# Kernel optimization log

Hardware: AMD Instinct MI355X
Metric: run time of the kernel (lower is better)

## Reference

```python
import math
import jax, jax.numpy as jnp
import numpy as np

B, C, NH, H, W = 8, 512, 4, 64, 64
CH = C // 8          # qkv channels = 64
HC = CH // NH        # head channels = 16


def _pos_encoding(c, h, w):
    # Faithful to torch code, including the raw memory reinterpretation of
    # pos_h (h, c) -> (1, c, h, 1) and pos_w (c//2, 2w) -> (1, c, 1, w).
    ph = jnp.arange(h, dtype=jnp.float32)[:, None]            # (h, 1)
    pw = jnp.arange(w, dtype=jnp.float32)[None, :]            # (1, w)
    div = jnp.exp(jnp.arange(0, c, 2, dtype=jnp.float32) * (-(math.log(10000.0) / c)))
    pos_h = ph * div[None, :]                                  # (h, c/2)
    pos_w = pw * div[:, None]                                  # (c/2, w)
    pos_h = jnp.concatenate([jnp.sin(pos_h), jnp.cos(pos_h)], axis=1)  # (h, c)
    pos_w = jnp.concatenate([jnp.sin(pos_w), jnp.cos(pos_w)], axis=1)  # (c/2, 2w)
    pos_h = pos_h.reshape(1, c, h, 1)   # raw view, as in torch
    pos_w = pos_w.reshape(1, c, 1, w)   # raw view, as in torch
    return pos_h + pos_w                # (1, c, h, w)


def _conv1x1(x, w, b):
    return jnp.einsum('bchw,oc->bohw', x, w) + b[None, :, None, None]


def setup_inputs() -> dict:
    key = jax.random.key(0)
    ks = jax.random.split(key, 6)
    s = 0.02
    return {
        'x':  jax.random.normal(ks[0], (B, C, H, W), dtype=jnp.float32),
        'wq': jax.random.normal(ks[1], (CH, C), dtype=jnp.float32) * s,
        'bq': jnp.zeros((CH,), dtype=jnp.float32),
        'wk': jax.random.normal(ks[2], (CH, C), dtype=jnp.float32) * s,
        'bk': jnp.zeros((CH,), dtype=jnp.float32),
        'wv': jax.random.normal(ks[3], (CH, C), dtype=jnp.float32) * s,
        'bv': jnp.zeros((CH,), dtype=jnp.float32),
        'wo': jax.random.normal(ks[4], (C, CH), dtype=jnp.float32) * s,
        'bo': jnp.zeros((C,), dtype=jnp.float32),
        'gamma': jnp.full((1,), 0.5, dtype=jnp.float32),  # nonzero to exercise whole graph
    }


def reference(x, wq, bq, wk, bk, wv, bv, wo, bo, gamma):
    b, c, h, w = x.shape
    nh, hc = NH, HC
    x = x + _pos_encoding(c, h, w)

    q = _conv1x1(x, wq, bq).reshape(b, nh, hc, h, w)
    k = _conv1x1(x, wk, bk).reshape(b, nh, hc, h, w)
    v = _conv1x1(x, wv, bv).reshape(b, nh, hc, h, w)

    # column (H) and row (W) views
    q_H = q.transpose(0, 1, 4, 2, 3).reshape(b * nh * w, hc, h).transpose(0, 2, 1)  # (bnw, h, hc)
    q_W = q.transpose(0, 1, 3, 2, 4).reshape(b * nh * h, hc, w).transpose(0, 2, 1)  # (bnh, w, hc)
    k_H = k.transpose(0, 1, 4, 2, 3).reshape(b * nh * w, hc, h)
    k_W = k.transpose(0, 1, 3, 2, 4).reshape(b * nh * h, hc, w)
    v_H = v.transpose(0, 1, 4, 2, 3).reshape(b * nh * w, hc, h)
    v_W = v.transpose(0, 1, 3, 2, 4).reshape(b * nh * h, hc, w)

    inf_mask = jnp.where(jnp.eye(h, dtype=bool), -jnp.inf, 0.0).astype(x.dtype)  # (h, h)
    energy_H = (jnp.matmul(q_H, k_H) + inf_mask[None]).reshape(b, nh, w, h, h).transpose(0, 2, 1, 3, 4)  # (b,w,nh,h,h)
    energy_W = jnp.matmul(q_W, k_W).reshape(b, nh, h, w, w).transpose(0, 2, 1, 3, 4)                     # (b,h,nh,w,w)

    conc = jax.nn.softmax(jnp.concatenate([energy_H, energy_W], axis=4), axis=4)  # (b,w,nh,h,h+w)

    att_H = conc[..., :h].transpose(0, 2, 1, 3, 4).reshape(b * nh * w, h, h)
    # NOTE: faithful to torch: (b,h,nh,w,w) is flattened in (b,h,nh) order
    att_W = conc[..., h:h + w].reshape(b * nh * h, w, w)

    out_H = jnp.matmul(v_H, att_H.transpose(0, 2, 1))
    out_H = out_H.reshape(b, nh, w, hc, h).transpose(0, 3, 4, 1, 2).reshape(b, nh * hc, h, w)
    out_W = jnp.matmul(v_W, att_W.transpose(0, 2, 1))
    out_W = out_W.reshape(b, nh, h, hc, w).transpose(0, 3, 1, 4, 2).reshape(b, nh * hc, h, w)

    out = _conv1x1(out_H + out_W, wo, bo)
    return gamma * out + x
```

## Files before the change

kernel.cpp:

```cpp
#include <hip/hip_runtime.h>
#include <math.h>


typedef unsigned int u32;
typedef unsigned short u16;
typedef __attribute__((ext_vector_type(8))) short short8;
typedef __attribute__((ext_vector_type(4))) float f32x4;

__device__ __forceinline__ u16 f2bf(float v) {
    u32 u = __float_as_uint(v);
    u32 r = (u + 0x7FFFu + ((u >> 16) & 1u)) >> 16;
    return (u16)r;
}

__device__ __forceinline__ float bf2f(u16 v) {
    return __uint_as_float(((u32)v) << 16);
}

__device__ __forceinline__ void gll16(const void* g, void* l) {
    __builtin_amdgcn_global_load_lds(
        (const __attribute__((address_space(1))) u32*)g,
        (__attribute__((address_space(3))) u32*)l, 16, 0, 0);
}

__global__ __launch_bounds__(64) void pos_kernel(float* __restrict__ PH,
                                                 float* __restrict__ PW) {
    const float r = 0.03597789207798663f;
    int c = blockIdx.x;
    int t = threadIdx.x;
    int i = c >> 3;
    int j = ((c & 7) << 6) | t;
    float ph;
    if (j < 256) ph = sinf((float)i * expf(-(float)j * r));
    else         ph = cosf((float)i * expf(-(float)(j - 256) * r));
    PH[c * 64 + t] = ph;
    int tt = c >> 1;
    float dv = expf(-(float)tt * r);
    PW[c * 64 + t] = (c & 1) ? cosf((float)t * dv) : sinf((float)t * dv);
}

__global__ __launch_bounds__(256) void wconv_kernel(
    const float* __restrict__ wq, const float* __restrict__ wk,
    const float* __restrict__ wv, const float* __restrict__ wo,
    u16* __restrict__ WT, u16* __restrict__ WOb) {
    int i = blockIdx.x * 256 + threadIdx.x;
    if (i < 98304) {
        float v;
        if (i < 32768)      v = wq[i];
        else if (i < 65536) v = wk[i - 32768];
        else                v = wv[i - 65536];
        WT[i] = f2bf(v);
    } else {
        WOb[i - 98304] = f2bf(wo[i - 98304]);
    }
}

__global__ __launch_bounds__(256) void wpos_kernel(
    const float* __restrict__ wq, const float* __restrict__ wk,
    const float* __restrict__ wv,
    const float* __restrict__ PH, const float* __restrict__ PW,
    float* __restrict__ WPH3, float* __restrict__ WPW3) {
    int gid = blockIdx.x * 256 + threadIdx.x;
    int h = gid & 63;
    int m = (gid >> 6) & 63;
    int t = gid >> 12;
    int mg = t >> 1, tbl = t & 1;
    const float* W = (mg == 0) ? wq : (mg == 1) ? wk : wv;
    const float* P = tbl ? PW : PH;
    const float* wr = W + m * 512;
    float s = 0.f;
#pragma unroll 8
    for (int c = 0; c < 512; ++c) s += wr[c] * P[c * 64 + h];
    (tbl ? WPW3 : WPH3)[(mg * 64 + m) * 64 + h] = s;
}

__global__ __launch_bounds__(512, 4) void qkvx_kernel(
    const float* __restrict__ x, const u16* __restrict__ WT,
    const float* __restrict__ bq, const float* __restrict__ bk,
    const float* __restrict__ bv,
    const float* __restrict__ WPH3, const float* __restrict__ WPW3,
    u16* __restrict__ Qc, u16* __restrict__ Kc, u16* __restrict__ Vc) {
    __shared__ u16 Wb[192 * 64];
    __shared__ u16 Bb[64 * 64];
    int L  = blockIdx.x;
    int b  = L & 7;
    int pt = L >> 3;
    int tid  = threadIdx.x;
    int w    = tid >> 6;
    int lane = tid & 63;
    int ln15 = lane & 15, quad = lane >> 4;
    int wm = w >> 2;
    int wp = w & 3;

    f32x4 acc[6];
#pragma unroll
    for (int i = 0; i < 6; ++i) acc[i] = (f32x4){0.f, 0.f, 0.f, 0.f};

    const float* xb = x + (size_t)b * 2097152 + pt * 64;
    int tp  = tid & 63;
    int tcc = tid >> 6;

    for (int kc = 0; kc < 512; kc += 64) {
        __syncthreads();
#pragma unroll
        for (int it = 0; it < 3; ++it) {
            int idx = tid + it * 512;
            int r = idx >> 3, s = idx & 7;
            gll16(WT + r * 512 + kc + ((s ^ (r & 7)) * 8), &Wb[idx * 8]);
        }
        {
            const float* xp = xb + (size_t)(kc + tcc * 8) * 4096 + tp;
            float v[8];
#pragma unroll
            for (int i = 0; i < 8; ++i) v[i] = xp[(size_t)i * 4096];
            short8 pk;
#pragma unroll
            for (int i = 0; i < 8; ++i) pk[i] = (short)f2bf(v[i]);
            *(short8*)&Bb[tp * 64 + ((tcc ^ (tp & 7)) * 8)] = pk;
        }
        __syncthreads();
#pragma unroll
        for (int ks = 0; ks < 2; ++ks) {
            int cs = ks * 4 + quad;
            int brow = wp * 16 + ln15;
            short8 bf = *(const short8*)&Bb[brow * 64 + ((cs ^ (brow & 7)) * 8)];
#pragma unroll
            for (int i = 0; i < 6; ++i) {
                int arow = (wm * 6 + i) * 16 + ln15;
                short8 af = *(const short8*)&Wb[arow * 64 + ((cs ^ (arow & 7)) * 8)];
                acc[i] = __builtin_amdgcn_mfma_f32_16x16x32_bf16(
                    af, bf, acc[i], 0, 0, 0);
            }
        }
    }

    int wc = wp * 16 + ln15;
#pragma unroll
    for (int i = 0; i < 6; ++i) {
        int mf = wm * 6 + i;
        int mg = mf >> 2, nm = mf & 3;
        const float* bias = (mg == 0) ? bq : (mg == 1) ? bk : bv;
        u16* T = (mg == 0) ? Qc : (mg == 1) ? Kc : Vc;
        float vals[4];
#pragma unroll
        for (int reg = 0; reg < 4; ++reg) {
            int m2 = nm * 16 + quad * 4 + reg;
            vals[reg] = acc[i][reg] + bias[m2]
                      + WPH3[(mg * 64 + m2) * 64 + pt]
                      + WPW3[(mg * 64 + m2) * 64 + wc];
        }
        ushort4 pk;
        pk.x = f2bf(vals[0]);
        pk.y = f2bf(vals[1]);
        pk.z = f2bf(vals[2]);
        pk.w = f2bf(vals[3]);
        *(ushort4*)&T[(((size_t)(b * 4 + nm) * 64 + pt) * 64 + wc) * 16
                      + quad * 4] = pk;
    }
}

__global__ __launch_bounds__(256, 4) void attn_kernel(
    const u16* __restrict__ Qc, const u16* __restrict__ Kc,
    const u16* __restrict__ Vc,
    u16* __restrict__ OHc, u16* __restrict__ OWc) {
    __shared__ u16 U[11008];
    u16* A_lds  = U;
    u16* B_lds  = U + 2560;
    u16* P_lds  = U;
    u16* VH_lds = U + 8704;
    u16* VW_lds = U + 9856;

    int b = blockIdx.x, n = blockIdx.y, a = blockIdx.z;
    int tid  = threadIdx.x;
    int w    = tid >> 6;
    int lane = tid & 63;
    int ln15 = lane & 15, quad = lane >> 4;
    int nv = a >> 4;
    int hv = ((a & 15) << 2) | n;

    const size_t cb = (((size_t)b * 4 + n) * 64 + a) * 1024;

    {
        int t = tid & 127;
        const short8 z8 = {0, 0, 0, 0, 0, 0, 0, 0};
        if (tid < 128) {
            int h = t >> 1, half = t & 1;
            size_t hb = (((size_t)b * 4 + n) * 64 + h) * 1024 + a * 16 + half * 8;
            short8 vA = *(const short8*)(Qc + hb);
            *(short8*)&A_lds[h * 40 + half * 8] = vA;
            short8 vK = *(const short8*)(Kc + hb);
            *(short8*)&B_lds[h * 48 + half * 8] = vK;
            *(short8*)&B_lds[h * 48 + 16 + half * 8] = z8;
            short8 vV = *(const short8*)(Vc + hb);
#pragma unroll
            for (int j = 0; j < 8; ++j)
                VH_lds[(half * 8 + j) * 72 + h] = (u16)vV[j];
        } else {
            short8 vA = *(const short8*)(Qc + cb + t * 8);
            *(short8*)&A_lds[(t >> 1) * 40 + 16 + (t & 1) * 8] = vA;
            short8 vK = *(const short8*)(Kc + cb + t * 8);
            *(short8*)&B_lds[(64 + (t >> 1)) * 48 + 16 + (t & 1) * 8] = vK;
            *(short8*)&B_lds[(64 + (t >> 1)) * 48 + (t & 1) * 8] = z8;
            size_t wb2 = (((size_t)b * 4 + nv) * 64 + hv) * 1024 + t * 8;
            short8 vV = *(const short8*)(Vc + wb2);
#pragma unroll
            for (int j = 0; j < 8; ++j)
                VW_lds[((t & 1) * 8 + j) * 72 + (t >> 1)] = (u16)vV[j];
        }
    }
    __syncthreads();

    const f32x4 zf = {0.f, 0.f, 0.f, 0.f};
    short8 af = *(const short8*)&A_lds[(w * 16 + ln15) * 40 + quad * 8];
    f32x4 acc[8];
#pragma unroll
    for (int nt = 0; nt < 8; ++nt) {
        short8 bf = *(const short8*)&B_lds[(nt * 16 + ln15) * 48 + quad * 8];
        acc[nt] = __builtin_amdgcn_mfma_f32_16x16x32_bf16(af, bf, zf, 0, 0, 0);
    }

#pragma unroll
    for (int nt = 0; nt < 4; ++nt)
#pragma unroll
        for (int r = 0; r < 4; ++r)
            if (nt * 16 + ln15 == w * 16 + quad * 4 + r) acc[nt][r] = -1e30f;

    float inv[4];
#pragma unroll
    for (int r = 0; r < 4; ++r) {
        float mrow = acc[0][r];
#pragma unroll
        for (int nt = 1; nt < 8; ++nt) mrow = fmaxf(mrow, acc[nt][r]);
        mrow = fmaxf(mrow, __shfl_xor(mrow, 1, 64));
        mrow = fmaxf(mrow, __shfl_xor(mrow, 2, 64));
        mrow = fmaxf(mrow, __shfl_xor(mrow, 4, 64));
        mrow = fmaxf(mrow, __shfl_xor(mrow, 8, 64));
        float s = 0.f;
#pragma unroll
        for (int nt = 0; nt < 8; ++nt) {
            float e = __expf(acc[nt][r] - mrow);
            acc[nt][r] = e;
            s += e;
        }
        s += __shfl_xor(s, 1, 64);
        s += __shfl_xor(s, 2, 64);
        s += __shfl_xor(s, 4, 64);
        s += __shfl_xor(s, 8, 64);
        inv[r] = 1.0f / s;
    }
    __syncthreads();
#pragma unroll
    for (int nt = 0; nt < 8; ++nt)
#pragma unroll
        for (int r = 0; r < 4; ++r)
            P_lds[(w * 16 + quad * 4 + r) * 136 + nt * 16 + ln15] =
                f2bf(acc[nt][r] * inv[r]);
    __syncthreads();

    int prow = (w * 16 + ln15) * 136;
    short8 a0 = *(const short8*)&P_lds[prow +       quad * 8];
    short8 a1 = *(const short8*)&P_lds[prow + 32  + quad * 8];
    short8 a2 = *(const short8*)&P_lds[prow + 64  + quad * 8];
    short8 a3 = *(const short8*)&P_lds[prow + 96  + quad * 8];
    short8 b0 = *(const short8*)&VH_lds[ln15 * 72 +      quad * 8];
    short8 b1 = *(const short8*)&VH_lds[ln15 * 72 + 32 + quad * 8];
    short8 c0 = *(const short8*)&VW_lds[ln15 * 72 +      quad * 8];
    short8 c1 = *(const short8*)&VW_lds[ln15 * 72 + 32 + quad * 8];
    f32x4 oH = __builtin_amdgcn_mfma_f32_16x16x32_bf16(a0, b0, zf, 0, 0, 0);
    oH = __builtin_amdgcn_mfma_f32_16x16x32_bf16(a1, b1, oH, 0, 0, 0);
    f32x4 oW = __builtin_amdgcn_mfma_f32_16x16x32_bf16(a2, c0, zf, 0, 0, 0);
    oW = __builtin_amdgcn_mfma_f32_16x16x32_bf16(a3, c1, oW, 0, 0, 0);

    __syncthreads();
    u16* eph = U;
    u16* epw = U + 16 * 68;
#pragma unroll
    for (int r = 0; r < 4; ++r) {
        eph[(quad * 4 + r) * 68 + ln15 * 4 + w]   = f2bf(oH[r]);
        epw[(w * 16 + quad * 4 + r) * 20 + ln15]  = f2bf(oW[r]);
    }
    __syncthreads();
    {
        int t = tid;
        ushort4 vh = *(const ushort4*)&eph[(t >> 4) * 68 + (t & 15) * 4];
        ushort4 vw = *(const ushort4*)&epw[(t >> 2) * 20 + (t & 3) * 4];
        size_t cbase = (((size_t)b * 4 + n) * 64 + a) * 1024;
        *(ushort4*)&OHc[cbase + t * 4] = vh;
        *(ushort4*)&OWc[cbase + t * 4] = vw;
    }
}

__global__ __launch_bounds__(256) void sconv_kernel(
    const u16* __restrict__ OHc, const u16* __restrict__ OWc,
    u16* __restrict__ Sb) {
    int b = blockIdx.x;
    int h = blockIdx.y;
    int t  = threadIdx.x;
    int wp = t >> 2;
    int cq = t & 3;

    const u16* ohp = OHc + ((((size_t)b * 4 + (h & 3)) * 64 + wp) * 1024
                            + (h >> 2) * 64 + cq * 16);
    short8 oh0 = *(const short8*)ohp;
    short8 oh1 = *(const short8*)(ohp + 8);

    const u16* owb = OWc + (((size_t)b * 4 + (wp & 3)) * 64) * 1024 + h * 16 + cq * 4;
    ushort4 owv[4];
#pragma unroll
    for (int nvi = 0; nvi < 4; ++nvi)
        owv[nvi] = *(const ushort4*)(owb + (size_t)((nvi << 4) | (wp >> 2)) * 1024);

    u16 res[16];
#pragma unroll
    for (int j = 0; j < 16; ++j) {
        u16 ohv = (j < 8) ? (u16)oh0[j] : (u16)oh1[j - 8];
        const ushort4& q = owv[j & 3];
        u16 owu = (j >> 2) == 0 ? q.x : (j >> 2) == 1 ? q.y : (j >> 2) == 2 ? q.z : q.w;
        res[j] = f2bf(bf2f(ohv) + bf2f(owu));
    }
    u16* dst = Sb + (((size_t)b * 4096 + h * 64 + wp) * 64 + cq * 16);
    *(short8*)dst       = *(short8*)&res[0];
    *(short8*)(dst + 8) = *(short8*)&res[8];
}

__global__ __launch_bounds__(256, 4) void finalm_kernel(
    const u16* __restrict__ Sb, const u16* __restrict__ WOb,
    const float* __restrict__ bo, const float* __restrict__ gamma,
    const float* __restrict__ x, const float* __restrict__ PH,
    const float* __restrict__ PW, float* __restrict__ out) {
    __shared__ u16 Ab[64 * 64];
    __shared__ u16 Bb[128 * 64];
    int pt = blockIdx.x;
    int mc = blockIdx.y;
    int b  = blockIdx.z;
    int tid  = threadIdx.x;
    int w    = tid >> 6;
    int lane = tid & 63;
    int ln15 = lane & 15, quad = lane >> 4;
    int p0 = pt * 128, m0 = mc * 64;

    float4 xv[4][2];
#pragma unroll
    for (int mf = 0; mf < 4; ++mf) {
        int m = m0 + mf * 16 + ln15;
#pragma unroll
        for (int pf = 0; pf < 2; ++pf) {
            int pb = p0 + w * 32 + pf * 16 + quad * 4;
            xv[mf][pf] = *(const float4*)&x[((size_t)(b * 512 + m)) * 4096 + pb];
        }
    }

    const u16* Ag = WOb + m0 * 64;
    const u16* Sg = Sb + ((size_t)b * 4096 + p0) * 64;

#pragma unroll
    for (int it = 0; it < 2; ++it) {
        int idx = tid + it * 256;
        int r = idx >> 3, s = idx & 7;
        gll16(Ag + r * 64 + ((s ^ (r & 7)) * 8), &Ab[idx * 8]);
    }
#pragma unroll
    for (int it = 0; it < 4; ++it) {
        int idx = tid + it * 256;
        int r = idx >> 3, s = idx & 7;
        gll16(Sg + r * 64 + ((s ^ (r & 7)) * 8), &Bb[idx * 8]);
    }
    __syncthreads();

    const f32x4 zf = {0.f, 0.f, 0.f, 0.f};
    f32x4 acc[4][2];
#pragma unroll
    for (int mf = 0; mf < 4; ++mf)
#pragma unroll
        for (int pf = 0; pf < 2; ++pf)
            acc[mf][pf] = zf;
#pragma unroll
    for (int ks = 0; ks < 2; ++ks) {
        int cs = ks * 4 + quad;
        short8 af[2], bf[4];
#pragma unroll
        for (int pf = 0; pf < 2; ++pf) {
            int row = w * 32 + pf * 16 + ln15;
            af[pf] = *(const short8*)&Bb[row * 64 + ((cs ^ (row & 7)) * 8)];
        }
#pragma unroll
        for (int mf = 0; mf < 4; ++mf) {
            int row = mf * 16 + ln15;
            bf[mf] = *(const short8*)&Ab[row * 64 + ((cs ^ (row & 7)) * 8)];
        }
#pragma unroll
        for (int mf = 0; mf < 4; ++mf)
#pragma unroll
            for (int pf = 0; pf < 2; ++pf)
                acc[mf][pf] = __builtin_amdgcn_mfma_f32_16x16x32_bf16(
                    af[pf], bf[mf], acc[mf][pf], 0, 0, 0);
    }

    float g = gamma[0];
    int h = pt * 2 + (w >> 1);
    int plb = (w & 1) * 32;
#pragma unroll
    for (int mf = 0; mf < 4; ++mf) {
        int m = m0 + mf * 16 + ln15;
        float bm = bo[m];
        float ph = PH[m * 64 + h];
#pragma unroll
        for (int pf = 0; pf < 2; ++pf) {
            int pb = p0 + w * 32 + pf * 16 + quad * 4;
            size_t o = ((size_t)(b * 512 + m)) * 4096 + pb;
            float4 pwv = *(const float4*)&PW[m * 64 + plb + pf * 16 + quad * 4];
            float4 res;
            res.x = g * (acc[mf][pf][0] + bm) + xv[mf][pf].x + ph + pwv.x;
            res.y = g * (acc[mf][pf][1] + bm) + xv[mf][pf].y + ph + pwv.y;
            res.z = g * (acc[mf][pf][2] + bm) + xv[mf][pf].z + ph + pwv.z;
            res.w = g * (acc[mf][pf][3] + bm) + xv[mf][pf].w + ph + pwv.w;
            *(float4*)&out[o] = res;
        }
    }
}

extern "C" void kernel_launch(void* const* d_in, const int* in_sizes, int n_in,
                              void* d_out, int out_size, void* d_ws, size_t ws_size,
                              hipStream_t stream) {
    const float* x     = (const float*)d_in[0];
    const float* wq    = (const float*)d_in[1];
    const float* bq    = (const float*)d_in[2];
    const float* wk    = (const float*)d_in[3];
    const float* bk    = (const float*)d_in[4];
    const float* wv    = (const float*)d_in[5];
    const float* bv    = (const float*)d_in[6];
    const float* wo    = (const float*)d_in[7];
    const float* bo    = (const float*)d_in[8];
    const float* gamma = (const float*)d_in[9];
    float* out = (float*)d_out;
    float* ws  = (float*)d_ws;

    float* PH   = ws;
    float* PW   = PH + 32768;
    float* WPH3 = PW + 32768;
    float* WPW3 = WPH3 + 12288;
    u16*   WT   = (u16*)(WPW3 + 12288);
    u16*   WOb  = WT + 98304;
    u16*   Qc   = WOb + 32768;
    u16*   Kc   = Qc + 2097152;
    u16*   Vc   = Kc + 2097152;
    u16*   OHc  = Vc + 2097152;
    u16*   OWc  = OHc + 2097152;
    u16*   Sbb  = OWc + 2097152;

    pos_kernel<<<dim3(512), dim3(64), 0, stream>>>(PH, PW);
    wconv_kernel<<<dim3(512), dim3(256), 0, stream>>>(wq, wk, wv, wo, WT, WOb);
    wpos_kernel<<<dim3(96), dim3(256), 0, stream>>>(wq, wk, wv, PH, PW, WPH3, WPW3);
    qkvx_kernel<<<dim3(512), dim3(512), 0, stream>>>(
        x, WT, bq, bk, bv, WPH3, WPW3, Qc, Kc, Vc);
    attn_kernel<<<dim3(8, 4, 64), dim3(256), 0, stream>>>(
        Qc, Kc, Vc, OHc, OWc);
    sconv_kernel<<<dim3(8, 64), dim3(256), 0, stream>>>(OHc, OWc, Sbb);
    finalm_kernel<<<dim3(32, 8, 8), dim3(256), 0, stream>>>(
        Sbb, WOb, bo, gamma, x, PH, PW, out);
}
```

Before: 197.2 us.

## Fuse head-sum into final projection and merge prep kernels

Result: no change. 196.6 us (-0.3%).

```diff
diff --git a/kernel.cpp b/kernel.cpp
--- a/kernel.cpp
+++ b/kernel.cpp
@@ -23,35 +23,37 @@
         (__attribute__((address_space(3))) u32*)l, 16, 0, 0);
 }
 
-__global__ __launch_bounds__(64) void pos_kernel(float* __restrict__ PH,
-                                                 float* __restrict__ PW) {
-    const float r = 0.03597789207798663f;
-    int c = blockIdx.x;
-    int t = threadIdx.x;
-    int i = c >> 3;
-    int j = ((c & 7) << 6) | t;
-    float ph;
-    if (j < 256) ph = sinf((float)i * expf(-(float)j * r));
-    else         ph = cosf((float)i * expf(-(float)(j - 256) * r));
-    PH[c * 64 + t] = ph;
-    int tt = c >> 1;
-    float dv = expf(-(float)tt * r);
-    PW[c * 64 + t] = (c & 1) ? cosf((float)t * dv) : sinf((float)t * dv);
-}
-
-__global__ __launch_bounds__(256) void wconv_kernel(
+__global__ __launch_bounds__(256) void prep_kernel(
     const float* __restrict__ wq, const float* __restrict__ wk,
     const float* __restrict__ wv, const float* __restrict__ wo,
+    float* __restrict__ PH, float* __restrict__ PW,
     u16* __restrict__ WT, u16* __restrict__ WOb) {
-    int i = blockIdx.x * 256 + threadIdx.x;
-    if (i < 98304) {
-        float v;
-        if (i < 32768)      v = wq[i];
-        else if (i < 65536) v = wk[i - 32768];
-        else                v = wv[i - 65536];
-        WT[i] = f2bf(v);
+    int blk = blockIdx.x;
+    int tid = threadIdx.x;
+    if (blk < 128) {
+        int gid = blk * 256 + tid;
+        int c = gid >> 6, t = gid & 63;
+        const float r = 0.03597789207798663f;
+        int i = c >> 3;
+        int j = ((c & 7) << 6) | t;
+        float ph;
+        if (j < 256) ph = sinf((float)i * expf(-(float)j * r));
+        else         ph = cosf((float)i * expf(-(float)(j - 256) * r));
+        PH[c * 64 + t] = ph;
+        int tt = c >> 1;
+        float dv = expf(-(float)tt * r);
+        PW[c * 64 + t] = (c & 1) ? cosf((float)t * dv) : sinf((float)t * dv);
     } else {
-        WOb[i - 98304] = f2bf(wo[i - 98304]);
+        int i = (blk - 128) * 256 + tid;
+        if (i < 98304) {
+            float v;
+            if (i < 32768)      v = wq[i];
+            else if (i < 65536) v = wk[i - 32768];
+            else                v = wv[i - 65536];
+            WT[i] = f2bf(v);
+        } else {
+            WOb[i - 98304] = f2bf(wo[i - 98304]);
+        }
     }
 }
 
@@ -290,41 +292,9 @@
     }
 }
 
-__global__ __launch_bounds__(256) void sconv_kernel(
+__global__ __launch_bounds__(256, 4) void finalm_kernel(
     const u16* __restrict__ OHc, const u16* __restrict__ OWc,
-    u16* __restrict__ Sb) {
-    int b = blockIdx.x;
-    int h = blockIdx.y;
-    int t  = threadIdx.x;
-    int wp = t >> 2;
-    int cq = t & 3;
-
-    const u16* ohp = OHc + ((((size_t)b * 4 + (h & 3)) * 64 + wp) * 1024
-                            + (h >> 2) * 64 + cq * 16);
-    short8 oh0 = *(const short8*)ohp;
-    short8 oh1 = *(const short8*)(ohp + 8);
-
-    const u16* owb = OWc + (((size_t)b * 4 + (wp & 3)) * 64) * 1024 + h * 16 + cq * 4;
-    ushort4 owv[4];
-#pragma unroll
-    for (int nvi = 0; nvi < 4; ++nvi)
-        owv[nvi] = *(const ushort4*)(owb + (size_t)((nvi << 4) | (wp >> 2)) * 1024);
-
-    u16 res[16];
-#pragma unroll
-    for (int j = 0; j < 16; ++j) {
-        u16 ohv = (j < 8) ? (u16)oh0[j] : (u16)oh1[j - 8];
-        const ushort4& q = owv[j & 3];
-        u16 owu = (j >> 2) == 0 ? q.x : (j >> 2) == 1 ? q.y : (j >> 2) == 2 ? q.z : q.w;
-        res[j] = f2bf(bf2f(ohv) + bf2f(owu));
-    }
-    u16* dst = Sb + (((size_t)b * 4096 + h * 64 + wp) * 64 + cq * 16);
-    *(short8*)dst       = *(short8*)&res[0];
-    *(short8*)(dst + 8) = *(short8*)&res[8];
-}
-
-__global__ __launch_bounds__(256, 4) void finalm_kernel(
-    const u16* __restrict__ Sb, const u16* __restrict__ WOb,
+    const u16* __restrict__ WOb,
     const float* __restrict__ bo, const float* __restrict__ gamma,
     const float* __restrict__ x, const float* __restrict__ PH,
     const float* __restrict__ PW, float* __restrict__ out) {
@@ -351,19 +321,56 @@
     }
 
     const u16* Ag = WOb + m0 * 64;
-    const u16* Sg = Sb + ((size_t)b * 4096 + p0) * 64;
-
 #pragma unroll
     for (int it = 0; it < 2; ++it) {
         int idx = tid + it * 256;
         int r = idx >> 3, s = idx & 7;
         gll16(Ag + r * 64 + ((s ^ (r & 7)) * 8), &Ab[idx * 8]);
     }
-#pragma unroll
-    for (int it = 0; it < 4; ++it) {
-        int idx = tid + it * 256;
-        int r = idx >> 3, s = idx & 7;
-        gll16(Sg + r * 64 + ((s ^ (r & 7)) * 8), &Bb[idx * 8]);
+
+    {
+        int pairI = tid >> 1;
+        int hLoc  = pairI >> 6;
+        int wp    = pairI & 63;
+        int cHalf = tid & 1;
+        int h     = pt * 2 + hLoc;
+        int r     = hLoc * 64 + wp;
+        const u16* ohp = OHc + ((((size_t)b * 4 + (h & 3)) * 64 + wp) * 1024
+                                + (h >> 2) * 64 + cHalf * 32);
+        short8 oh0 = *(const short8*)(ohp);
+        short8 oh1 = *(const short8*)(ohp + 8);
+        short8 oh2 = *(const short8*)(ohp + 16);
+        short8 oh3 = *(const short8*)(ohp + 24);
+        u16 res[32];
+#pragma unroll
+        for (int half = 0; half < 2; ++half) {
+            int cq = cHalf * 2 + half;
+            const u16* owb = OWc + (((size_t)b * 4 + (wp & 3)) * 64) * 1024
+                           + h * 16 + cq * 4;
+            ushort4 owv[4];
+#pragma unroll
+            for (int nvi = 0; nvi < 4; ++nvi)
+                owv[nvi] = *(const ushort4*)(owb
+                             + (size_t)((nvi << 4) | (wp >> 2)) * 1024);
+#pragma unroll
+            for (int j = 0; j < 16; ++j) {
+                int idx = half * 16 + j;
+                u16 ohv;
+                if (idx < 8)       ohv = (u16)oh0[idx];
+                else if (idx < 16) ohv = (u16)oh1[idx - 8];
+                else if (idx < 24) ohv = (u16)oh2[idx - 16];
+                else               ohv = (u16)oh3[idx - 24];
+                const ushort4& q = owv[j & 3];
+                u16 owu = (j >> 2) == 0 ? q.x : (j >> 2) == 1 ? q.y
+                        : (j >> 2) == 2 ? q.z : q.w;
+                res[idx] = f2bf(bf2f(ohv) + bf2f(owu));
+            }
+        }
+#pragma unroll
+        for (int k = 0; k < 4; ++k) {
+            int s = cHalf * 4 + k;
+            *(short8*)&Bb[r * 64 + ((s ^ (r & 7)) * 8)] = *(short8*)&res[k * 8];
+        }
     }
     __syncthreads();
 
@@ -446,16 +453,14 @@
     u16*   Vc   = Kc + 2097152;
     u16*   OHc  = Vc + 2097152;
     u16*   OWc  = OHc + 2097152;
-    u16*   Sbb  = OWc + 2097152;
-
-    pos_kernel<<<dim3(512), dim3(64), 0, stream>>>(PH, PW);
-    wconv_kernel<<<dim3(512), dim3(256), 0, stream>>>(wq, wk, wv, wo, WT, WOb);
+
+    prep_kernel<<<dim3(640), dim3(256), 0, stream>>>(
+        wq, wk, wv, wo, PH, PW, WT, WOb);
     wpos_kernel<<<dim3(96), dim3(256), 0, stream>>>(wq, wk, wv, PH, PW, WPH3, WPW3);
     qkvx_kernel<<<dim3(512), dim3(512), 0, stream>>>(
         x, WT, bq, bk, bv, WPH3, WPW3, Qc, Kc, Vc);
     attn_kernel<<<dim3(8, 4, 64), dim3(256), 0, stream>>>(
         Qc, Kc, Vc, OHc, OWc);
-    sconv_kernel<<<dim3(8, 64), dim3(256), 0, stream>>>(OHc, OWc, Sbb);
     finalm_kernel<<<dim3(32, 8, 8), dim3(256), 0, stream>>>(
-        Sbb, WOb, bo, gamma, x, PH, PW, out);
-}
+        OHc, OWc, WOb, bo, gamma, x, PH, PW, out);
+}
```
